# Kernel optimization log

Hardware: AMD Instinct MI355X
Metric: run time of the kernel (lower is better)

## Reference

```python
import jax, jax.numpy as jnp
import numpy as np

MOMENTUM = 0.99
EPS = 1e-08


def setup_inputs() -> dict:
    key = jax.random.key(0)
    k1, = jax.random.split(key, 1)
    B, F, T = 32, 257, 3000
    mag = jax.random.uniform(k1, (B, F, T), dtype=jnp.float32)  # magnitudes >= 0
    bias = jnp.zeros((1,), dtype=jnp.float32)
    running_mean = jnp.ones((1,), dtype=jnp.float32)
    return {"mag": mag, "bias": bias, "running_mean": running_mean}


def reference(mag, bias, running_mean):
    """Causal per-frame EMA energy normalization (eval-mode sequence path).

    mag: [B, F, T] -> (mag_norm [B, F, T], mag_mean [B, 1, T])
    """
    B, F, T = mag.shape
    frame_means = mag.mean(axis=1)          # [B, T]
    init = jnp.broadcast_to(running_mean, (B,))  # m_0 = running_mean per batch

    def step(carry, fm_t):
        m = MOMENTUM * carry + (1.0 - MOMENTUM) * fm_t  # [B]
        return m, m

    _, means = jax.lax.scan(step, init, frame_means.T)  # means: [T, B]
    mean_with_bias = means.T + bias[0]                  # [B, T]
    mag_norm = mag / (mean_with_bias[:, None, :] + EPS)  # [B, F, T]
    mag_mean = mean_with_bias[:, None, :]               # [B, 1, T]
    return mag_norm, mag_mean
```

## Files before the change

kernel.cpp:

```cpp
#include <hip/hip_runtime.h>


#define B_   32
#define F_   257
#define T_   3000
#define T4   750
#define NG1  16
#define MOM  0.99f
#define OMM  0.01f
#define EPS_ 1e-8f
#define INVF (1.0f / 257.0f)

#define ACC4(a, v) { a.x += v.x; a.y += v.y; a.z += v.z; a.w += v.w; }

__global__ __launch_bounds__(256) void k1_partial(const float* __restrict__ mag,
                                                  float* __restrict__ partial) {
    const int blk = blockIdx.x;
    const int b   = blk >> 4;
    const int g   = blk & 15;
    const int tid = threadIdx.x;
    const bool has2 = tid < (T4 - 512);

    const float4* magv = reinterpret_cast<const float4*>(mag)
                       + ((size_t)(b * F_ + g * 16)) * T4;
    float4 a0 = make_float4(0.f,0.f,0.f,0.f);
    float4 a1 = make_float4(0.f,0.f,0.f,0.f);
    float4 a2 = make_float4(0.f,0.f,0.f,0.f);

    #pragma unroll 4
    for (int r = 0; r < 16; ++r) {
        const float4* row = magv + (size_t)r * T4;
        float4 v0 = row[tid];
        float4 v1 = row[tid + 256];
        ACC4(a0, v0);
        ACC4(a1, v1);
        if (has2) { float4 v2 = row[tid + 512]; ACC4(a2, v2); }
    }
    if (g == 15) {
        const float4* row = magv + (size_t)16 * T4;
        float4 v0 = row[tid];
        float4 v1 = row[tid + 256];
        ACC4(a0, v0);
        ACC4(a1, v1);
        if (has2) { float4 v2 = row[tid + 512]; ACC4(a2, v2); }
    }

    float4* pv = reinterpret_cast<float4*>(partial) + (size_t)blk * T4;
    pv[tid]       = a0;
    pv[tid + 256] = a1;
    if (has2) pv[tid + 512] = a2;
}

__global__ __launch_bounds__(256) void k_reduce_scan(const float* __restrict__ src,
                                                     int nrows,
                                                     const float* __restrict__ bias,
                                                     const float* __restrict__ rmean,
                                                     float* __restrict__ recip,
                                                     float* __restrict__ mag_mean) {
    __shared__ float4 xs4[T4];
    float* xs = reinterpret_cast<float*>(xs4);
    __shared__ float sA[256];
    __shared__ float sB[256];

    const int b   = blockIdx.x;
    const int tid = threadIdx.x;
    const bool has2 = tid < (T4 - 512);

    {
        const float4* sv = reinterpret_cast<const float4*>(src)
                         + (size_t)b * nrows * T4;
        float4 a0 = make_float4(0.f,0.f,0.f,0.f);
        float4 a1 = make_float4(0.f,0.f,0.f,0.f);
        float4 a2 = make_float4(0.f,0.f,0.f,0.f);
        #pragma unroll 4
        for (int r = 0; r < nrows; ++r) {
            const float4* row = sv + (size_t)r * T4;
            float4 v0 = row[tid];
            float4 v1 = row[tid + 256];
            ACC4(a0, v0);
            ACC4(a1, v1);
            if (has2) { float4 v2 = row[tid + 512]; ACC4(a2, v2); }
        }
        a0.x *= INVF; a0.y *= INVF; a0.z *= INVF; a0.w *= INVF;
        a1.x *= INVF; a1.y *= INVF; a1.z *= INVF; a1.w *= INVF;
        xs4[tid]       = a0;
        xs4[tid + 256] = a1;
        if (has2) {
            a2.x *= INVF; a2.y *= INVF; a2.z *= INVF; a2.w *= INVF;
            xs4[tid + 512] = a2;
        }
    }
    __syncthreads();

    const int CH = 12;
    const int t0 = tid * CH;
    float A = 1.f, Bv = 0.f;
    if (t0 < T_) {
        #pragma unroll
        for (int j = 0; j < CH; ++j) {
            Bv = MOM * Bv + OMM * xs[t0 + j];
            A *= MOM;
        }
    }
    sA[tid] = A; sB[tid] = Bv;
    __syncthreads();

    for (int off = 1; off < 256; off <<= 1) {
        float cA = sA[tid], cB = sB[tid];
        float pA = 1.f, pB = 0.f;
        if (tid >= off) { pA = sA[tid - off]; pB = sB[tid - off]; }
        __syncthreads();
        if (tid >= off) { sA[tid] = pA * cA; sB[tid] = pB * cA + cB; }
        __syncthreads();
    }

    float pA = 1.f, pB = 0.f;
    if (tid > 0) { pA = sA[tid - 1]; pB = sB[tid - 1]; }
    __syncthreads();

    const float bias0 = bias[0];
    if (t0 < T_) {
        float m = pA * rmean[0] + pB;
        #pragma unroll
        for (int j = 0; j < CH; ++j) {
            m = MOM * m + OMM * xs[t0 + j];
            xs[t0 + j] = m + bias0;
        }
    }
    __syncthreads();

    float4* mmv = reinterpret_cast<float4*>(mag_mean) + (size_t)b * T4;
    float4* rcv = reinterpret_cast<float4*>(recip)    + (size_t)b * T4;
    for (int i = tid; i < T4; i += 256) {
        float4 v = xs4[i];
        mmv[i] = v;
        float4 rv;
        rv.x = 1.0f / (v.x + EPS_); rv.y = 1.0f / (v.y + EPS_);
        rv.z = 1.0f / (v.z + EPS_); rv.w = 1.0f / (v.w + EPS_);
        rcv[i] = rv;
    }
}

__global__ __launch_bounds__(256) void k3_norm(const float* __restrict__ mag,
                                               const float* __restrict__ recip,
                                               float* __restrict__ out) {
    __shared__ float4 rec4[T4];
    const int blk = blockIdx.x;
    const int b   = blk / 33;
    const int ch  = blk % 33;
    const int tid = threadIdx.x;

    {
        const float4* rcv = reinterpret_cast<const float4*>(recip) + (size_t)b * T4;
        for (int i = tid; i < T4; i += 256) rec4[i] = rcv[i];
    }
    __syncthreads();

    const bool has2 = tid < (T4 - 512);
    const float4 r0 = rec4[tid];
    const float4 r1 = rec4[tid + 256];
    const float4 r2 = has2 ? rec4[tid + 512] : r0;

    const int f0 = ch * 8;
    const int nr = (ch == 32) ? 1 : 8;
    const float4* magv = reinterpret_cast<const float4*>(mag)
                       + ((size_t)(b * F_ + f0)) * T4;
    float4* ov = reinterpret_cast<float4*>(out)
               + ((size_t)(b * F_ + f0)) * T4;

    for (int r = 0; r < nr; ++r) {
        const float4* row = magv + (size_t)r * T4;
        float4*       orow = ov  + (size_t)r * T4;
        float4 v0 = row[tid];
        float4 v1 = row[tid + 256];
        float4 o;
        o.x = v0.x * r0.x; o.y = v0.y * r0.y; o.z = v0.z * r0.z; o.w = v0.w * r0.w;
        orow[tid] = o;
        o.x = v1.x * r1.x; o.y = v1.y * r1.y; o.z = v1.z * r1.z; o.w = v1.w * r1.w;
        orow[tid + 256] = o;
        if (has2) {
            float4 v2 = row[tid + 512];
            o.x = v2.x * r2.x; o.y = v2.y * r2.y; o.z = v2.z * r2.z; o.w = v2.w * r2.w;
            orow[tid + 512] = o;
        }
    }
}

extern "C" void kernel_launch(void* const* d_in, const int* in_sizes, int n_in,
                              void* d_out, int out_size, void* d_ws, size_t ws_size,
                              hipStream_t stream) {
    (void)in_sizes; (void)n_in; (void)out_size;
    const float* mag   = (const float*)d_in[0];
    const float* bias  = (const float*)d_in[1];
    const float* rmean = (const float*)d_in[2];
    float* out      = (float*)d_out;
    float* mag_mean = out + (size_t)B_ * F_ * T_;

    float* recip = (float*)d_ws;
    const size_t recip_sz   = (size_t)B_ * T_ * sizeof(float);
    const size_t partial_sz = (size_t)B_ * NG1 * T_ * sizeof(float);

    if (ws_size >= recip_sz + partial_sz) {
        float* partial = recip + (size_t)B_ * T_;
        k1_partial<<<B_ * NG1, 256, 0, stream>>>(mag, partial);
        k_reduce_scan<<<B_, 256, 0, stream>>>(partial, NG1, bias, rmean,
                                              recip, mag_mean);
    } else {
        k_reduce_scan<<<B_, 256, 0, stream>>>(mag, F_, bias, rmean,
                                              recip, mag_mean);
    }
    k3_norm<<<B_ * 33, 256, 0, stream>>>(mag, recip, out);
}
```

Measured before the change: 206.4 us.

## Fuse reduce, scan and normalize into one persistent kernel with flag sync

Replaces the three-kernel pipeline with one kernel of 1024 blocks. Each block loads its 8 rows of mag into registers, writes partial column sums, and signals a per-block flag. The ch==0 block of each batch waits on those flags, does the reduction and EMA scan, then publishes the reciprocals. The other blocks spin on a per-batch flag and normalize straight from registers, so mag is read from HBM only once and two launches disappear. The costs are 96 float4 registers per thread, which may cause spills or low occupancy, and a cross-block spin wait that relies on every block being co-resident to avoid deadlock.

After: 597.0 us. 189% more time.

```diff
diff --git a/kernel.cpp b/kernel.cpp
--- a/kernel.cpp
+++ b/kernel.cpp
@@ -5,13 +5,199 @@
 #define F_   257
 #define T_   3000
 #define T4   750
-#define NG1  16
 #define MOM  0.99f
 #define OMM  0.01f
 #define EPS_ 1e-8f
 #define INVF (1.0f / 257.0f)
 
 #define ACC4(a, v) { a.x += v.x; a.y += v.y; a.z += v.z; a.w += v.w; }
+
+__device__ inline void wait_flag(const unsigned* p) {
+    while (__hip_atomic_load(p, __ATOMIC_ACQUIRE, __HIP_MEMORY_SCOPE_AGENT) == 0u)
+        __builtin_amdgcn_s_sleep(4);
+}
+
+__global__ __launch_bounds__(256) void ema_onepass(
+    const float* __restrict__ mag,
+    const float* __restrict__ bias,
+    const float* __restrict__ rmean,
+    float* __restrict__ out,
+    float* __restrict__ mag_mean,
+    unsigned* __restrict__ flag1,
+    unsigned* __restrict__ flag2,
+    float* __restrict__ partial,
+    float* __restrict__ recip)
+{
+    __shared__ float4 xs4[T4];
+    float* xs = reinterpret_cast<float*>(xs4);
+    __shared__ float sA[256];
+    __shared__ float sB[256];
+
+    const int blk = blockIdx.x;
+    const int b   = blk >> 5;
+    const int ch  = blk & 31;
+    const int tid = threadIdx.x;
+    const bool c2 = tid < (T4 - 512);
+
+    const float4* magv = reinterpret_cast<const float4*>(mag)
+                       + (size_t)(b * F_ + ch * 8) * T4;
+    float4 r[8][3];
+    float4 a0 = make_float4(0.f,0.f,0.f,0.f);
+    float4 a1 = make_float4(0.f,0.f,0.f,0.f);
+    float4 a2 = make_float4(0.f,0.f,0.f,0.f);
+    #pragma unroll
+    for (int i = 0; i < 8; ++i) {
+        r[i][0] = magv[(size_t)i * T4 + tid];
+        r[i][1] = magv[(size_t)i * T4 + tid + 256];
+        ACC4(a0, r[i][0]);
+        ACC4(a1, r[i][1]);
+        if (c2) { r[i][2] = magv[(size_t)i * T4 + tid + 512]; ACC4(a2, r[i][2]); }
+    }
+    if (ch == 31) {
+        float4 v0 = magv[(size_t)8 * T4 + tid];
+        float4 v1 = magv[(size_t)8 * T4 + tid + 256];
+        ACC4(a0, v0); ACC4(a1, v1);
+        if (c2) { float4 v2 = magv[(size_t)8 * T4 + tid + 512]; ACC4(a2, v2); }
+    }
+
+    {
+        float4* pv = reinterpret_cast<float4*>(partial) + (size_t)blk * T4;
+        pv[tid]       = a0;
+        pv[tid + 256] = a1;
+        if (c2) pv[tid + 512] = a2;
+    }
+    __syncthreads();
+    if (tid == 0)
+        __hip_atomic_store(&flag1[blk], 1u, __ATOMIC_RELEASE,
+                           __HIP_MEMORY_SCOPE_AGENT);
+
+    if (ch == 0) {
+        if (tid < 32) wait_flag(&flag1[b * 32 + tid]);
+        __syncthreads();
+
+        const float4* pv = reinterpret_cast<const float4*>(partial)
+                         + (size_t)b * 32 * T4;
+        float4 s0 = make_float4(0.f,0.f,0.f,0.f);
+        float4 s1 = make_float4(0.f,0.f,0.f,0.f);
+        float4 s2 = make_float4(0.f,0.f,0.f,0.f);
+        #pragma unroll 4
+        for (int j = 0; j < 32; ++j) {
+            const float4* rp = pv + (size_t)j * T4;
+            float4 v0 = rp[tid];
+            float4 v1 = rp[tid + 256];
+            ACC4(s0, v0); ACC4(s1, v1);
+            if (c2) { float4 v2 = rp[tid + 512]; ACC4(s2, v2); }
+        }
+        s0.x *= INVF; s0.y *= INVF; s0.z *= INVF; s0.w *= INVF;
+        s1.x *= INVF; s1.y *= INVF; s1.z *= INVF; s1.w *= INVF;
+        xs4[tid]       = s0;
+        xs4[tid + 256] = s1;
+        if (c2) {
+            s2.x *= INVF; s2.y *= INVF; s2.z *= INVF; s2.w *= INVF;
+            xs4[tid + 512] = s2;
+        }
+        __syncthreads();
+
+        const int CH = 12;
+        const int t0 = tid * CH;
+        float A = 1.f, Bv = 0.f;
+        if (t0 < T_) {
+            #pragma unroll
+            for (int j = 0; j < CH; ++j) {
+                Bv = MOM * Bv + OMM * xs[t0 + j];
+                A *= MOM;
+            }
+        }
+        sA[tid] = A; sB[tid] = Bv;
+        __syncthreads();
+
+        for (int off = 1; off < 256; off <<= 1) {
+            float cA = sA[tid], cB = sB[tid];
+            float pA = 1.f, pB = 0.f;
+            if (tid >= off) { pA = sA[tid - off]; pB = sB[tid - off]; }
+            __syncthreads();
+            if (tid >= off) { sA[tid] = pA * cA; sB[tid] = pB * cA + cB; }
+            __syncthreads();
+        }
+        float pA = 1.f, pB = 0.f;
+        if (tid > 0) { pA = sA[tid - 1]; pB = sB[tid - 1]; }
+        __syncthreads();
+
+        const float bias0 = bias[0];
+        if (t0 < T_) {
+            float m = pA * rmean[0] + pB;
+            #pragma unroll
+            for (int j = 0; j < CH; ++j) {
+                m = MOM * m + OMM * xs[t0 + j];
+                xs[t0 + j] = m + bias0;
+            }
+        }
+        __syncthreads();
+
+        float4* mmv = reinterpret_cast<float4*>(mag_mean) + (size_t)b * T4;
+        float4* rcv = reinterpret_cast<float4*>(recip)    + (size_t)b * T4;
+        for (int i = tid; i < T4; i += 256) {
+            float4 v = xs4[i];
+            mmv[i] = v;
+            float4 rv;
+            rv.x = 1.0f / (v.x + EPS_); rv.y = 1.0f / (v.y + EPS_);
+            rv.z = 1.0f / (v.z + EPS_); rv.w = 1.0f / (v.w + EPS_);
+            rcv[i] = rv;
+            xs4[i] = rv;
+        }
+        __syncthreads();
+        if (tid == 0)
+            __hip_atomic_store(&flag2[b], 1u, __ATOMIC_RELEASE,
+                               __HIP_MEMORY_SCOPE_AGENT);
+    }
+
+    float4 rc0, rc1, rc2;
+    if (ch == 0) {
+        rc0 = xs4[tid];
+        rc1 = xs4[tid + 256];
+        rc2 = c2 ? xs4[tid + 512] : rc0;
+    } else {
+        if (tid == 0) wait_flag(&flag2[b]);
+        __syncthreads();
+        const float4* rcv = reinterpret_cast<const float4*>(recip) + (size_t)b * T4;
+        rc0 = rcv[tid];
+        rc1 = rcv[tid + 256];
+        rc2 = c2 ? rcv[tid + 512] : rc0;
+    }
+
+    float4* ov = reinterpret_cast<float4*>(out) + (size_t)(b * F_ + ch * 8) * T4;
+    #pragma unroll
+    for (int i = 0; i < 8; ++i) {
+        float4 o;
+        float4 v0 = r[i][0];
+        o.x = v0.x * rc0.x; o.y = v0.y * rc0.y; o.z = v0.z * rc0.z; o.w = v0.w * rc0.w;
+        ov[(size_t)i * T4 + tid] = o;
+        float4 v1 = r[i][1];
+        o.x = v1.x * rc1.x; o.y = v1.y * rc1.y; o.z = v1.z * rc1.z; o.w = v1.w * rc1.w;
+        ov[(size_t)i * T4 + tid + 256] = o;
+        if (c2) {
+            float4 v2 = r[i][2];
+            o.x = v2.x * rc2.x; o.y = v2.y * rc2.y; o.z = v2.z * rc2.z; o.w = v2.w * rc2.w;
+            ov[(size_t)i * T4 + tid + 512] = o;
+        }
+    }
+    if (ch == 31) {
+        float4 o;
+        float4 v0 = magv[(size_t)8 * T4 + tid];
+        o.x = v0.x * rc0.x; o.y = v0.y * rc0.y; o.z = v0.z * rc0.z; o.w = v0.w * rc0.w;
+        ov[(size_t)8 * T4 + tid] = o;
+        float4 v1 = magv[(size_t)8 * T4 + tid + 256];
+        o.x = v1.x * rc1.x; o.y = v1.y * rc1.y; o.z = v1.z * rc1.z; o.w = v1.w * rc1.w;
+        ov[(size_t)8 * T4 + tid + 256] = o;
+        if (c2) {
+            float4 v2 = magv[(size_t)8 * T4 + tid + 512];
+            o.x = v2.x * rc2.x; o.y = v2.y * rc2.y; o.z = v2.z * rc2.z; o.w = v2.w * rc2.w;
+            ov[(size_t)8 * T4 + tid + 512] = o;
+        }
+    }
+}
+
+#define NG1  16
 
 __global__ __launch_bounds__(256) void k1_partial(const float* __restrict__ mag,
                                                   float* __restrict__ partial) {
@@ -32,19 +218,16 @@
         const float4* row = magv + (size_t)r * T4;
         float4 v0 = row[tid];
         float4 v1 = row[tid + 256];
-        ACC4(a0, v0);
-        ACC4(a1, v1);
+        ACC4(a0, v0); ACC4(a1, v1);
         if (has2) { float4 v2 = row[tid + 512]; ACC4(a2, v2); }
     }
     if (g == 15) {
         const float4* row = magv + (size_t)16 * T4;
         float4 v0 = row[tid];
         float4 v1 = row[tid + 256];
-        ACC4(a0, v0);
-        ACC4(a1, v1);
+        ACC4(a0, v0); ACC4(a1, v1);
         if (has2) { float4 v2 = row[tid + 512]; ACC4(a2, v2); }
     }
-
     float4* pv = reinterpret_cast<float4*>(partial) + (size_t)blk * T4;
     pv[tid]       = a0;
     pv[tid + 256] = a1;
@@ -77,8 +260,7 @@
             const float4* row = sv + (size_t)r * T4;
             float4 v0 = row[tid];
             float4 v1 = row[tid + 256];
-            ACC4(a0, v0);
-            ACC4(a1, v1);
+            ACC4(a0, v0); ACC4(a1, v1);
             if (has2) { float4 v2 = row[tid + 512]; ACC4(a2, v2); }
         }
         a0.x *= INVF; a0.y *= INVF; a0.z *= INVF; a0.w *= INVF;
@@ -113,7 +295,6 @@
         if (tid >= off) { sA[tid] = pA * cA; sB[tid] = pB * cA + cB; }
         __syncthreads();
     }
-
     float pA = 1.f, pB = 0.f;
     if (tid > 0) { pA = sA[tid - 1]; pB = sB[tid - 1]; }
     __syncthreads();
@@ -169,8 +350,8 @@
                + ((size_t)(b * F_ + f0)) * T4;
 
     for (int r = 0; r < nr; ++r) {
-        const float4* row = magv + (size_t)r * T4;
-        float4*       orow = ov  + (size_t)r * T4;
+        const float4* row  = magv + (size_t)r * T4;
+        float4*       orow = ov   + (size_t)r * T4;
         float4 v0 = row[tid];
         float4 v1 = row[tid + 256];
         float4 o;
@@ -196,6 +377,24 @@
     float* out      = (float*)d_out;
     float* mag_mean = out + (size_t)B_ * F_ * T_;
 
+    const size_t flags_bytes   = 8192;
+    const size_t partial_elems = (size_t)B_ * 32 * T_;
+    const size_t recip_elems   = (size_t)B_ * T_;
+    const size_t need_onepass  = flags_bytes
+                               + partial_elems * sizeof(float)
+                               + recip_elems * sizeof(float);
+
+    if (ws_size >= need_onepass) {
+        unsigned* flag1 = (unsigned*)d_ws;
+        unsigned* flag2 = flag1 + 1024;
+        float* partial  = (float*)((char*)d_ws + flags_bytes);
+        float* recip    = partial + partial_elems;
+        hipMemsetAsync(d_ws, 0, flags_bytes, stream);
+        ema_onepass<<<B_ * 32, 256, 0, stream>>>(mag, bias, rmean, out, mag_mean,
+                                                 flag1, flag2, partial, recip);
+        return;
+    }
+
     float* recip = (float*)d_ws;
     const size_t recip_sz   = (size_t)B_ * T_ * sizeof(float);
     const size_t partial_sz = (size_t)B_ * NG1 * T_ * sizeof(float);
```

## Fuse partial reduction, EMA scan, and normalization into one kernel

Applied to the files above, without the earlier changes.

Replaces the separate reduce-scan kernel (32 blocks) and normalization kernel with a single kernel in which each of the B*33 blocks re-reduces the per-batch partial sums, redoes the EMA scan in shared memory, and applies the reciprocal directly. This removes one kernel launch, the low-parallelism scan kernel and the recip workspace round trip. In exchange, every block redundantly reads 16 partial rows and repeats the scan, adding cache traffic and latency before the streaming phase.

New measurement: 207.1 us. No clear change (+0.3%).

```diff
diff --git a/kernel.cpp b/kernel.cpp
--- a/kernel.cpp
+++ b/kernel.cpp
@@ -49,6 +49,128 @@
     pv[tid]       = a0;
     pv[tid + 256] = a1;
     if (has2) pv[tid + 512] = a2;
+}
+
+__global__ __launch_bounds__(256) void k2_scan_norm(
+    const float* __restrict__ partial,
+    const float* __restrict__ bias,
+    const float* __restrict__ rmean,
+    const float* __restrict__ mag,
+    float* __restrict__ out,
+    float* __restrict__ mag_mean)
+{
+    __shared__ float4 xs4[T4];
+    float* xs = reinterpret_cast<float*>(xs4);
+    __shared__ float sA[256];
+    __shared__ float sB[256];
+
+    const int blk = blockIdx.x;
+    const int b   = blk / 33;
+    const int ch  = blk % 33;
+    const int tid = threadIdx.x;
+    const bool c2 = tid < (T4 - 512);
+
+    {
+        const float4* pv = reinterpret_cast<const float4*>(partial)
+                         + (size_t)b * NG1 * T4;
+        float4 s0 = make_float4(0.f,0.f,0.f,0.f);
+        float4 s1 = make_float4(0.f,0.f,0.f,0.f);
+        float4 s2 = make_float4(0.f,0.f,0.f,0.f);
+        #pragma unroll 4
+        for (int r = 0; r < NG1; ++r) {
+            const float4* rp = pv + (size_t)r * T4;
+            float4 v0 = rp[tid];
+            float4 v1 = rp[tid + 256];
+            ACC4(s0, v0);
+            ACC4(s1, v1);
+            if (c2) { float4 v2 = rp[tid + 512]; ACC4(s2, v2); }
+        }
+        s0.x *= INVF; s0.y *= INVF; s0.z *= INVF; s0.w *= INVF;
+        s1.x *= INVF; s1.y *= INVF; s1.z *= INVF; s1.w *= INVF;
+        xs4[tid]       = s0;
+        xs4[tid + 256] = s1;
+        if (c2) {
+            s2.x *= INVF; s2.y *= INVF; s2.z *= INVF; s2.w *= INVF;
+            xs4[tid + 512] = s2;
+        }
+    }
+    __syncthreads();
+
+    const int CH = 12;
+    const int t0 = tid * CH;
+    float A = 1.f, Bv = 0.f;
+    if (t0 < T_) {
+        #pragma unroll
+        for (int j = 0; j < CH; ++j) {
+            Bv = MOM * Bv + OMM * xs[t0 + j];
+            A *= MOM;
+        }
+    }
+    sA[tid] = A; sB[tid] = Bv;
+    __syncthreads();
+
+    for (int off = 1; off < 256; off <<= 1) {
+        float cA = sA[tid], cB = sB[tid];
+        float pA = 1.f, pB = 0.f;
+        if (tid >= off) { pA = sA[tid - off]; pB = sB[tid - off]; }
+        __syncthreads();
+        if (tid >= off) { sA[tid] = pA * cA; sB[tid] = pB * cA + cB; }
+        __syncthreads();
+    }
+    float pA = 1.f, pB = 0.f;
+    if (tid > 0) { pA = sA[tid - 1]; pB = sB[tid - 1]; }
+    __syncthreads();
+
+    const float bias0 = bias[0];
+    if (t0 < T_) {
+        float m = pA * rmean[0] + pB;
+        #pragma unroll
+        for (int j = 0; j < CH; ++j) {
+            m = MOM * m + OMM * xs[t0 + j];
+            xs[t0 + j] = m + bias0;
+        }
+    }
+    __syncthreads();
+
+    if (ch == 0) {
+        float4* mmv = reinterpret_cast<float4*>(mag_mean) + (size_t)b * T4;
+        for (int i = tid; i < T4; i += 256) mmv[i] = xs4[i];
+    }
+    for (int i = tid; i < T4; i += 256) {
+        float4 v = xs4[i];
+        v.x = 1.0f / (v.x + EPS_); v.y = 1.0f / (v.y + EPS_);
+        v.z = 1.0f / (v.z + EPS_); v.w = 1.0f / (v.w + EPS_);
+        xs4[i] = v;
+    }
+    __syncthreads();
+
+    const float4 r0 = xs4[tid];
+    const float4 r1 = xs4[tid + 256];
+    const float4 r2 = c2 ? xs4[tid + 512] : r0;
+
+    const int f0 = ch * 8;
+    const int nr = (ch == 32) ? 1 : 8;
+    const float4* magv = reinterpret_cast<const float4*>(mag)
+                       + ((size_t)(b * F_ + f0)) * T4;
+    float4* ov = reinterpret_cast<float4*>(out)
+               + ((size_t)(b * F_ + f0)) * T4;
+
+    for (int r = 0; r < nr; ++r) {
+        const float4* row  = magv + (size_t)r * T4;
+        float4*       orow = ov   + (size_t)r * T4;
+        float4 v0 = row[tid];
+        float4 v1 = row[tid + 256];
+        float4 o;
+        o.x = v0.x * r0.x; o.y = v0.y * r0.y; o.z = v0.z * r0.z; o.w = v0.w * r0.w;
+        orow[tid] = o;
+        o.x = v1.x * r1.x; o.y = v1.y * r1.y; o.z = v1.z * r1.z; o.w = v1.w * r1.w;
+        orow[tid + 256] = o;
+        if (c2) {
+            float4 v2 = row[tid + 512];
+            o.x = v2.x * r2.x; o.y = v2.y * r2.y; o.z = v2.z * r2.z; o.w = v2.w * r2.w;
+            orow[tid + 512] = o;
+        }
+    }
 }
 
 __global__ __launch_bounds__(256) void k_reduce_scan(const float* __restrict__ src,
@@ -77,8 +199,7 @@
             const float4* row = sv + (size_t)r * T4;
             float4 v0 = row[tid];
             float4 v1 = row[tid + 256];
-            ACC4(a0, v0);
-            ACC4(a1, v1);
+            ACC4(a0, v0); ACC4(a1, v1);
             if (has2) { float4 v2 = row[tid + 512]; ACC4(a2, v2); }
         }
         a0.x *= INVF; a0.y *= INVF; a0.z *= INVF; a0.w *= INVF;
@@ -113,7 +234,6 @@
         if (tid >= off) { sA[tid] = pA * cA; sB[tid] = pB * cA + cB; }
         __syncthreads();
     }
-
     float pA = 1.f, pB = 0.f;
     if (tid > 0) { pA = sA[tid - 1]; pB = sB[tid - 1]; }
     __syncthreads();
@@ -169,8 +289,8 @@
                + ((size_t)(b * F_ + f0)) * T4;
 
     for (int r = 0; r < nr; ++r) {
-        const float4* row = magv + (size_t)r * T4;
-        float4*       orow = ov  + (size_t)r * T4;
+        const float4* row  = magv + (size_t)r * T4;
+        float4*       orow = ov   + (size_t)r * T4;
         float4 v0 = row[tid];
         float4 v1 = row[tid + 256];
         float4 o;
@@ -196,18 +316,18 @@
     float* out      = (float*)d_out;
     float* mag_mean = out + (size_t)B_ * F_ * T_;
 
-    float* recip = (float*)d_ws;
+    const size_t partial_sz = (size_t)B_ * NG1 * T_ * sizeof(float);
     const size_t recip_sz   = (size_t)B_ * T_ * sizeof(float);
-    const size_t partial_sz = (size_t)B_ * NG1 * T_ * sizeof(float);
-
-    if (ws_size >= recip_sz + partial_sz) {
-        float* partial = recip + (size_t)B_ * T_;
+
+    if (ws_size >= partial_sz) {
+        float* partial = (float*)d_ws;
         k1_partial<<<B_ * NG1, 256, 0, stream>>>(mag, partial);
-        k_reduce_scan<<<B_, 256, 0, stream>>>(partial, NG1, bias, rmean,
-                                              recip, mag_mean);
+        k2_scan_norm<<<B_ * 33, 256, 0, stream>>>(partial, bias, rmean, mag,
+                                                  out, mag_mean);
     } else {
+        float* recip = (float*)d_ws;
         k_reduce_scan<<<B_, 256, 0, stream>>>(mag, F_, bias, rmean,
                                               recip, mag_mean);
-    }
-    k3_norm<<<B_ * 33, 256, 0, stream>>>(mag, recip, out);
-}
+        k3_norm<<<B_ * 33, 256, 0, stream>>>(mag, recip, out);
+    }
+}
```

## Fuse scan into normalize kernel with redundant per-block scan, halve partial groups

Applied to the files above, without the earlier changes.

Merges the reduce/scan kernel and the normalization kernel into one. Each of 32 blocks per batch now redundantly reduces the partial sums and recomputes the EMA scan, then normalizes its own 8-row chunk from reciprocals held in shared memory. This removes a launch and the reciprocal round trip through global memory, and avoids the serial 32-block scan stage that left the GPU mostly idle. The partial-sum split drops from 16 to 8 row groups per batch to cut the redundant partial reads, at the cost of fewer blocks in the first kernel. The workspace-size fallback path is removed.

Measured after the change: 202.0 us. -2.1%, faster.

```diff
diff --git a/kernel.cpp b/kernel.cpp
--- a/kernel.cpp
+++ b/kernel.cpp
@@ -5,7 +5,7 @@
 #define F_   257
 #define T_   3000
 #define T4   750
-#define NG1  16
+#define NG1  8
 #define MOM  0.99f
 #define OMM  0.01f
 #define EPS_ 1e-8f
@@ -16,19 +16,19 @@
 __global__ __launch_bounds__(256) void k1_partial(const float* __restrict__ mag,
                                                   float* __restrict__ partial) {
     const int blk = blockIdx.x;
-    const int b   = blk >> 4;
-    const int g   = blk & 15;
+    const int b   = blk >> 3;
+    const int g   = blk & 7;
     const int tid = threadIdx.x;
     const bool has2 = tid < (T4 - 512);
 
     const float4* magv = reinterpret_cast<const float4*>(mag)
-                       + ((size_t)(b * F_ + g * 16)) * T4;
+                       + ((size_t)(b * F_ + g * 32)) * T4;
     float4 a0 = make_float4(0.f,0.f,0.f,0.f);
     float4 a1 = make_float4(0.f,0.f,0.f,0.f);
     float4 a2 = make_float4(0.f,0.f,0.f,0.f);
 
     #pragma unroll 4
-    for (int r = 0; r < 16; ++r) {
+    for (int r = 0; r < 32; ++r) {
         const float4* row = magv + (size_t)r * T4;
         float4 v0 = row[tid];
         float4 v1 = row[tid + 256];
@@ -36,8 +36,8 @@
         ACC4(a1, v1);
         if (has2) { float4 v2 = row[tid + 512]; ACC4(a2, v2); }
     }
-    if (g == 15) {
-        const float4* row = magv + (size_t)16 * T4;
+    if (g == 7) {
+        const float4* row = magv + (size_t)32 * T4;
         float4 v0 = row[tid];
         float4 v1 = row[tid + 256];
         ACC4(a0, v0);
@@ -51,43 +51,47 @@
     if (has2) pv[tid + 512] = a2;
 }
 
-__global__ __launch_bounds__(256) void k_reduce_scan(const float* __restrict__ src,
-                                                     int nrows,
-                                                     const float* __restrict__ bias,
-                                                     const float* __restrict__ rmean,
-                                                     float* __restrict__ recip,
-                                                     float* __restrict__ mag_mean) {
+__global__ __launch_bounds__(256) void k2_scan_norm(
+    const float* __restrict__ partial,
+    const float* __restrict__ bias,
+    const float* __restrict__ rmean,
+    const float* __restrict__ mag,
+    float* __restrict__ out,
+    float* __restrict__ mag_mean)
+{
     __shared__ float4 xs4[T4];
     float* xs = reinterpret_cast<float*>(xs4);
     __shared__ float sA[256];
     __shared__ float sB[256];
 
-    const int b   = blockIdx.x;
+    const int blk = blockIdx.x;
+    const int b   = blk >> 5;
+    const int ch  = blk & 31;
     const int tid = threadIdx.x;
-    const bool has2 = tid < (T4 - 512);
+    const bool c2 = tid < (T4 - 512);
 
     {
-        const float4* sv = reinterpret_cast<const float4*>(src)
-                         + (size_t)b * nrows * T4;
-        float4 a0 = make_float4(0.f,0.f,0.f,0.f);
-        float4 a1 = make_float4(0.f,0.f,0.f,0.f);
-        float4 a2 = make_float4(0.f,0.f,0.f,0.f);
-        #pragma unroll 4
-        for (int r = 0; r < nrows; ++r) {
-            const float4* row = sv + (size_t)r * T4;
-            float4 v0 = row[tid];
-            float4 v1 = row[tid + 256];
-            ACC4(a0, v0);
-            ACC4(a1, v1);
-            if (has2) { float4 v2 = row[tid + 512]; ACC4(a2, v2); }
+        const float4* pv = reinterpret_cast<const float4*>(partial)
+                         + (size_t)b * NG1 * T4;
+        float4 s0 = make_float4(0.f,0.f,0.f,0.f);
+        float4 s1 = make_float4(0.f,0.f,0.f,0.f);
+        float4 s2 = make_float4(0.f,0.f,0.f,0.f);
+        #pragma unroll
+        for (int r = 0; r < NG1; ++r) {
+            const float4* rp = pv + (size_t)r * T4;
+            float4 v0 = rp[tid];
+            float4 v1 = rp[tid + 256];
+            ACC4(s0, v0);
+            ACC4(s1, v1);
+            if (c2) { float4 v2 = rp[tid + 512]; ACC4(s2, v2); }
         }
-        a0.x *= INVF; a0.y *= INVF; a0.z *= INVF; a0.w *= INVF;
-        a1.x *= INVF; a1.y *= INVF; a1.z *= INVF; a1.w *= INVF;
-        xs4[tid]       = a0;
-        xs4[tid + 256] = a1;
-        if (has2) {
-            a2.x *= INVF; a2.y *= INVF; a2.z *= INVF; a2.w *= INVF;
-            xs4[tid + 512] = a2;
+        s0.x *= INVF; s0.y *= INVF; s0.z *= INVF; s0.w *= INVF;
+        s1.x *= INVF; s1.y *= INVF; s1.z *= INVF; s1.w *= INVF;
+        xs4[tid]       = s0;
+        xs4[tid + 256] = s1;
+        if (c2) {
+            s2.x *= INVF; s2.y *= INVF; s2.z *= INVF; s2.w *= INVF;
+            xs4[tid + 512] = s2;
         }
     }
     __syncthreads();
@@ -113,7 +117,6 @@
         if (tid >= off) { sA[tid] = pA * cA; sB[tid] = pB * cA + cB; }
         __syncthreads();
     }
-
     float pA = 1.f, pB = 0.f;
     if (tid > 0) { pA = sA[tid - 1]; pB = sB[tid - 1]; }
     __syncthreads();
@@ -129,48 +132,32 @@
     }
     __syncthreads();
 
-    float4* mmv = reinterpret_cast<float4*>(mag_mean) + (size_t)b * T4;
-    float4* rcv = reinterpret_cast<float4*>(recip)    + (size_t)b * T4;
+    if (ch == 0) {
+        float4* mmv = reinterpret_cast<float4*>(mag_mean) + (size_t)b * T4;
+        for (int i = tid; i < T4; i += 256) mmv[i] = xs4[i];
+    }
     for (int i = tid; i < T4; i += 256) {
         float4 v = xs4[i];
-        mmv[i] = v;
-        float4 rv;
-        rv.x = 1.0f / (v.x + EPS_); rv.y = 1.0f / (v.y + EPS_);
-        rv.z = 1.0f / (v.z + EPS_); rv.w = 1.0f / (v.w + EPS_);
-        rcv[i] = rv;
-    }
-}
-
-__global__ __launch_bounds__(256) void k3_norm(const float* __restrict__ mag,
-                                               const float* __restrict__ recip,
-                                               float* __restrict__ out) {
-    __shared__ float4 rec4[T4];
-    const int blk = blockIdx.x;
-    const int b   = blk / 33;
-    const int ch  = blk % 33;
-    const int tid = threadIdx.x;
-
-    {
-        const float4* rcv = reinterpret_cast<const float4*>(recip) + (size_t)b * T4;
-        for (int i = tid; i < T4; i += 256) rec4[i] = rcv[i];
+        v.x = 1.0f / (v.x + EPS_); v.y = 1.0f / (v.y + EPS_);
+        v.z = 1.0f / (v.z + EPS_); v.w = 1.0f / (v.w + EPS_);
+        xs4[i] = v;
     }
     __syncthreads();
 
-    const bool has2 = tid < (T4 - 512);
-    const float4 r0 = rec4[tid];
-    const float4 r1 = rec4[tid + 256];
-    const float4 r2 = has2 ? rec4[tid + 512] : r0;
+    const float4 r0 = xs4[tid];
+    const float4 r1 = xs4[tid + 256];
+    const float4 r2 = c2 ? xs4[tid + 512] : r0;
 
     const int f0 = ch * 8;
-    const int nr = (ch == 32) ? 1 : 8;
+    const int nr = (ch == 31) ? 9 : 8;
     const float4* magv = reinterpret_cast<const float4*>(mag)
                        + ((size_t)(b * F_ + f0)) * T4;
     float4* ov = reinterpret_cast<float4*>(out)
                + ((size_t)(b * F_ + f0)) * T4;
 
     for (int r = 0; r < nr; ++r) {
-        const float4* row = magv + (size_t)r * T4;
-        float4*       orow = ov  + (size_t)r * T4;
+        const float4* row  = magv + (size_t)r * T4;
+        float4*       orow = ov   + (size_t)r * T4;
         float4 v0 = row[tid];
         float4 v1 = row[tid + 256];
         float4 o;
@@ -178,7 +165,7 @@
         orow[tid] = o;
         o.x = v1.x * r1.x; o.y = v1.y * r1.y; o.z = v1.z * r1.z; o.w = v1.w * r1.w;
         orow[tid + 256] = o;
-        if (has2) {
+        if (c2) {
             float4 v2 = row[tid + 512];
             o.x = v2.x * r2.x; o.y = v2.y * r2.y; o.z = v2.z * r2.z; o.w = v2.w * r2.w;
             orow[tid + 512] = o;
@@ -189,25 +176,15 @@
 extern "C" void kernel_launch(void* const* d_in, const int* in_sizes, int n_in,
                               void* d_out, int out_size, void* d_ws, size_t ws_size,
                               hipStream_t stream) {
-    (void)in_sizes; (void)n_in; (void)out_size;
+    (void)in_sizes; (void)n_in; (void)out_size; (void)ws_size;
     const float* mag   = (const float*)d_in[0];
     const float* bias  = (const float*)d_in[1];
     const float* rmean = (const float*)d_in[2];
     float* out      = (float*)d_out;
     float* mag_mean = out + (size_t)B_ * F_ * T_;
 
-    float* recip = (float*)d_ws;
-    const size_t recip_sz   = (size_t)B_ * T_ * sizeof(float);
-    const size_t partial_sz = (size_t)B_ * NG1 * T_ * sizeof(float);
-
-    if (ws_size >= recip_sz + partial_sz) {
-        float* partial = recip + (size_t)B_ * T_;
-        k1_partial<<<B_ * NG1, 256, 0, stream>>>(mag, partial);
-        k_reduce_scan<<<B_, 256, 0, stream>>>(partial, NG1, bias, rmean,
-                                              recip, mag_mean);
-    } else {
-        k_reduce_scan<<<B_, 256, 0, stream>>>(mag, F_, bias, rmean,
-                                              recip, mag_mean);
-    }
-    k3_norm<<<B_ * 33, 256, 0, stream>>>(mag, recip, out);
+    float* partial = (float*)d_ws;
+    k1_partial<<<B_ * NG1, 256, 0, stream>>>(mag, partial);
+    k2_scan_norm<<<B_ * 32, 256, 0, stream>>>(partial, bias, rmean, mag,
+                                              out, mag_mean);
 }
```
